# Kernel optimization log

Measured on AMD Instinct MI355X. Metric: run time of the kernel, lower is better.

## Reference

```python
import jax, jax.numpy as jnp
import numpy as np

N_STATE = 64
N_LAYERS = 4
D_MODEL = 512
D_OUT = 256
BATCH = 16
SEQLEN = 2048


def setup_inputs() -> dict:
    key = jax.random.key(0)
    ks = jax.random.split(key, 16)
    H, N, nl = D_MODEL, N_STATE, N_LAYERS
    inp = {}
    inp["x"] = jax.random.normal(ks[0], (BATCH, SEQLEN, D_MODEL), dtype=jnp.float32)
    # encoder / decoder dense
    inp["enc_w"] = jax.random.normal(ks[1], (D_MODEL, D_MODEL), jnp.float32) / np.sqrt(D_MODEL)
    inp["enc_b"] = jnp.zeros((D_MODEL,), jnp.float32)
    inp["dec_w"] = jax.random.normal(ks[2], (D_MODEL, D_OUT), jnp.float32) / np.sqrt(D_MODEL)
    inp["dec_b"] = jnp.zeros((D_OUT,), jnp.float32)
    # per-layer LayerNorm
    inp["ln_scale"] = jnp.ones((nl, D_MODEL), jnp.float32)
    inp["ln_bias"] = jnp.zeros((nl, D_MODEL), jnp.float32)
    # per-layer S4 DPLR params (stored as real/imag float pairs)
    inp["lambda_re"] = -0.5 * jnp.ones((nl, H, N), jnp.float32)
    inp["lambda_im"] = jnp.broadcast_to(np.pi * jnp.arange(N, dtype=jnp.float32), (nl, H, N))
    inp["p_re"] = jax.random.normal(ks[3], (nl, H, N), jnp.float32) * 0.5
    inp["p_im"] = jax.random.normal(ks[4], (nl, H, N), jnp.float32) * 0.5
    inp["b_re"] = jax.random.normal(ks[5], (nl, H, N), jnp.float32) * 0.5
    inp["b_im"] = jax.random.normal(ks[6], (nl, H, N), jnp.float32) * 0.5
    inp["c_re"] = jax.random.normal(ks[7], (nl, H, N), jnp.float32) * 0.5
    inp["c_im"] = jax.random.normal(ks[8], (nl, H, N), jnp.float32) * 0.5
    inp["log_step"] = jax.random.uniform(ks[9], (nl, H), jnp.float32, minval=np.log(1e-3), maxval=np.log(1e-1))
    inp["d_param"] = jnp.ones((nl, H), jnp.float32)
    # per-layer output Dense
    inp["out_w"] = jax.random.normal(ks[10], (nl, D_MODEL, D_MODEL), jnp.float32) / np.sqrt(D_MODEL)
    inp["out_b"] = jnp.zeros((nl, D_MODEL), jnp.float32)
    return inp


def _layer_norm(x, scale, bias, eps=1e-6):
    mu = jnp.mean(x, axis=-1, keepdims=True)
    var = jnp.mean(jnp.square(x - mu), axis=-1, keepdims=True)
    return (x - mu) * jax.lax.rsqrt(var + eps) * scale + bias


def _kernel_dplr(Lam, P, B, C, step, L):
    # Lam,P,B,C: [H,N] complex64; step: [H] float32 -> K: [H,L] float32
    theta = (2.0 * np.pi / L) * jnp.arange(L, dtype=jnp.float32)
    Omega = jnp.exp(-1j * theta)                        # [L] roots of unity
    g = (2.0 / step)[:, None] * ((1.0 - Omega) / (1.0 + Omega))[None, :]  # [H,L]
    c = 2.0 / (1.0 + Omega)                             # [L]
    r = 1.0 / (g[:, :, None] - Lam[:, None, :])         # [H,L,N] resolvent (Cauchy)
    Cc, Pc = jnp.conj(C), jnp.conj(P)
    k00 = jnp.einsum("hn,hln->hl", Cc * B, r)
    k01 = jnp.einsum("hn,hln->hl", Cc * P, r)
    k10 = jnp.einsum("hn,hln->hl", Pc * B, r)
    k11 = jnp.einsum("hn,hln->hl", Pc * P, r)
    at_roots = c[None, :] * (k00 - k01 * (1.0 / (1.0 + k11)) * k10)  # [H,L]
    return jnp.fft.ifft(at_roots, n=L, axis=-1).real


def _s4_apply(u, Lam, P, B, C, step, D):
    # u: [Bt,L,H]; causal FFT convolution with kernel K[h,:] per channel
    L = u.shape[1]
    K = _kernel_dplr(Lam, P, B, C, step, L)             # [H,L]
    ud = jnp.fft.rfft(u, n=2 * L, axis=1)               # [Bt,L+1,H]
    Kd = jnp.fft.rfft(K, n=2 * L, axis=-1)              # [H,L+1]
    y = jnp.fft.irfft(ud * Kd.T[None], n=2 * L, axis=1)[:, :L]
    return y + D[None, None, :] * u


def reference(x, enc_w, enc_b, ln_scale, ln_bias, lambda_re, lambda_im,
              p_re, p_im, b_re, b_im, c_re, c_im, log_step, d_param,
              out_w, out_b, dec_w, dec_b):
    h = x @ enc_w + enc_b
    n_layers = ln_scale.shape[0]
    for i in range(n_layers):
        skip = h
        z = _layer_norm(h, ln_scale[i], ln_bias[i])
        Lam = lambda_re[i] + 1j * lambda_im[i]
        P = p_re[i] + 1j * p_im[i]
        B = b_re[i] + 1j * b_im[i]
        C = c_re[i] + 1j * c_im[i]
        z = _s4_apply(z, Lam, P, B, C, jnp.exp(log_step[i]), d_param[i])
        z = jax.nn.gelu(z)
        z = z @ out_w[i] + out_b[i]
        h = skip + z  # dropout=0.0 -> identity
    logits = h @ dec_w + dec_b
    return jax.nn.log_softmax(logits, axis=-1)
```

## Files before the change

### kernel.cpp

```cpp
#include <hip/hip_runtime.h>
#include <hip/hip_bf16.h>

#define NLAY 4
#define DH   512
#define NST  64
#define NB   16
#define SL   2048
#define NDO  256
#define BL   (NB*SL)
#define KDIM 512
#define TWOPI 6.283185307179586476925287

typedef unsigned short u16;
typedef __attribute__((ext_vector_type(8))) short  short8v;
typedef __attribute__((ext_vector_type(8))) unsigned short ushort8v;
typedef __attribute__((ext_vector_type(4))) float  f32x4;

#define RCPF(x) __builtin_amdgcn_rcpf(x)

__device__ __forceinline__ float bf2f(u16 v){
  union { unsigned u; float f; } x; x.u = ((unsigned)v) << 16; return x.f;
}
__device__ __forceinline__ u16 f2bf(float f){
  union { float f; unsigned u; } x; x.f = f;
  unsigned u = x.u;
  unsigned r = u + 0x7fffu + ((u >> 16) & 1u);
  return (u16)(r >> 16);
}
__device__ __forceinline__ void cmulw(float& xr, float& xi, float wr, float wi){
  float tr = xr*wr - xi*wi;
  xi = fmaf(xr, wi, xi*wr);
  xr = tr;
}
__device__ __forceinline__ float gelu_fast(float v){
  const float c0 = 0.7978845608028654f;
  float u = c0 * fmaf(0.044715f, v*v*v, v);
  return v * RCPF(1.0f + __expf(-2.0f * u));
}

template<int SGN>
__device__ __forceinline__ void dft4w(float& r0, float& i0, float& r1, float& i1,
                                      float& r2, float& i2, float& r3, float& i3){
  const float t0r = r0 + r2, t0i = i0 + i2;
  const float t1r = r0 - r2, t1i = i0 - i2;
  const float t2r = r1 + r3, t2i = i1 + i3;
  const float t3r = r1 - r3, t3i = i1 - i3;
  r0 = t0r + t2r; i0 = t0i + t2i;
  r2 = t0r - t2r; i2 = t0i - t2i;
  if (SGN < 0){ r1 = t1r + t3i; i1 = t1i - t3r; r3 = t1r - t3i; i3 = t1i + t3r; }
  else        { r1 = t1r - t3i; i1 = t1i + t3r; r3 = t1r + t3i; i3 = t1i - t3r; }
}

template<int SGN>
__device__ __forceinline__ void dft16(float* re, float* im){
#pragma unroll
  for (int b = 0; b < 4; b++)
    dft4w<SGN>(re[b], im[b], re[4+b], im[4+b], re[8+b], im[8+b], re[12+b], im[12+b]);
  const float C1 = 0.92387953251128675613f, S1_ = 0.38268343236508977172f;
  const float C2 = 0.70710678118654752440f;
  const float sg = (SGN < 0) ? -1.f : 1.f;
  cmulw(re[5],  im[5],   C1,  sg*S1_);
  cmulw(re[9],  im[9],   C2,  sg*C2);
  cmulw(re[13], im[13],  S1_, sg*C1);
  cmulw(re[6],  im[6],   C2,  sg*C2);
  cmulw(re[10], im[10],  0.f, sg*1.f);
  cmulw(re[14], im[14], -C2,  sg*C2);
  cmulw(re[7],  im[7],   S1_, sg*C1);
  cmulw(re[11], im[11], -C2,  sg*C2);
  cmulw(re[15], im[15], -C1,  sg*(-S1_));
#pragma unroll
  for (int c = 0; c < 4; c++)
    dft4w<SGN>(re[4*c], im[4*c], re[4*c+1], im[4*c+1], re[4*c+2], im[4*c+2], re[4*c+3], im[4*c+3]);
  float tr_, ti_;
#define SWP(A,B) tr_=re[A]; re[A]=re[B]; re[B]=tr_; ti_=im[A]; im[A]=im[B]; im[B]=ti_;
  SWP(1,4) SWP(2,8) SWP(3,12) SWP(6,9) SWP(7,13) SWP(11,14)
#undef SWP
}

__device__ __forceinline__ int cxpad(int i){ return i + (i >> 4) + ((i >> 8) << 1); }
#define CXSZ 4384

__device__ __forceinline__ void fwd4096(float* re, float* im, float2* cx, int t){
  dft16<-1>(re, im);
  const float a0 = -(float)(TWOPI/4096.0) * (float)t;
#pragma unroll
  for (int k = 0; k < 16; k++){
    if (k){ float sn = __sinf(a0*(float)k), cs = __cosf(a0*(float)k); cmulw(re[k], im[k], cs, sn); }
    cx[cxpad(t + 256*k)] = make_float2(re[k], im[k]);
  }
  __syncthreads();
  const int k1 = t >> 4, m2 = t & 15;
  const int b2 = k1*256 + m2;
#pragma unroll
  for (int j = 0; j < 16; j++){ float2 v = cx[cxpad(b2 + 16*j)]; re[j] = v.x; im[j] = v.y; }
  dft16<-1>(re, im);
  const float b0 = -(float)(TWOPI/256.0) * (float)m2;
#pragma unroll
  for (int k = 0; k < 16; k++){
    if (k){ float sn = __sinf(b0*(float)k), cs = __cosf(b0*(float)k); cmulw(re[k], im[k], cs, sn); }
    cx[cxpad(b2 + 16*k)] = make_float2(re[k], im[k]);
  }
  __syncthreads();
#pragma unroll
  for (int j = 0; j < 16; j++){ float2 v = cx[cxpad(16*t + j)]; re[j] = v.x; im[j] = v.y; }
  dft16<-1>(re, im);
}

__device__ __forceinline__ void inv4096(float* re, float* im, float2* cx, int t){
  dft16<1>(re, im);
#pragma unroll
  for (int j = 0; j < 16; j++) cx[cxpad(16*t + j)] = make_float2(re[j], im[j]);
  __syncthreads();
  const int k1 = t >> 4, m2 = t & 15;
  const int b2 = k1*256 + m2;
  const float b0 = (float)(TWOPI/256.0) * (float)m2;
#pragma unroll
  for (int k = 0; k < 16; k++){
    float2 v = cx[cxpad(b2 + 16*k)];
    re[k] = v.x; im[k] = v.y;
    if (k){ float sn = __sinf(b0*(float)k), cs = __cosf(b0*(float)k); cmulw(re[k], im[k], cs, sn); }
  }
  dft16<1>(re, im);
#pragma unroll
  for (int j = 0; j < 16; j++) cx[cxpad(b2 + 16*j)] = make_float2(re[j], im[j]);
  __syncthreads();
  const float a0 = (float)(TWOPI/4096.0) * (float)t;
#pragma unroll
  for (int k = 0; k < 16; k++){
    float2 v = cx[cxpad(t + 256*k)];
    re[k] = v.x; im[k] = v.y;
    if (k){ float sn = __sinf(a0*(float)k), cs = __cosf(a0*(float)k); cmulw(re[k], im[k], cs, sn); }
  }
  dft16<1>(re, im);
}

__global__ __launch_bounds__(256) void prep_k(
  const float* __restrict__ lam_re, const float* __restrict__ lam_im,
  const float* __restrict__ p_re,  const float* __restrict__ p_im,
  const float* __restrict__ b_re,  const float* __restrict__ b_im,
  const float* __restrict__ c_re,  const float* __restrict__ c_im,
  float4* __restrict__ cwA, float4* __restrict__ cwB, float* __restrict__ cwS)
{
  const int i = blockIdx.x * 256 + threadIdx.x;
  const float lr = lam_re[i], li = lam_im[i];
  const float pr = p_re[i],  pi = p_im[i];
  const float br = b_re[i],  bi = b_im[i];
  const float cr = c_re[i],  ci = c_im[i];
  cwA[i] = make_float4(lr, li, cr*br + ci*bi, cr*bi - ci*br);
  cwB[i] = make_float4(cr*pr + ci*pi, cr*pi - ci*pr, pr*br + pi*bi, pr*bi - pi*br);
  cwS[i] = pr*pr + pi*pi;
}

__global__ __launch_bounds__(256, 2) void cauchy_k(
    const float4* __restrict__ cwA, const float4* __restrict__ cwB,
    const float* __restrict__ cwS, const float* __restrict__ lstep,
    float2* __restrict__ Kd)
{
  const int t = threadIdx.x;
  const int h = blockIdx.y, lay = blockIdx.z;
  const int lb = blockIdx.x * 256 + t;
  const int wb = (lay*DH + h) * NST;
  const float tw0 = 2.0f * expf(-lstep[lay*DH + h]);

  float T0,T1,T2,T3, g0,g1,g2,g3;
  { float sn, cs;
    sincosf((float)(TWOPI/4096.0)*(float)(lb       ), &sn, &cs); T0 = sn*RCPF(cs); g0 = tw0*T0;
    sincosf((float)(TWOPI/4096.0)*(float)(lb +  512), &sn, &cs); T1 = sn*RCPF(cs); g1 = tw0*T1;
    sincosf((float)(TWOPI/4096.0)*(float)(lb + 1024), &sn, &cs); T2 = sn*RCPF(cs); g2 = tw0*T2;
    sincosf((float)(TWOPI/4096.0)*(float)(lb + 1536), &sn, &cs); T3 = sn*RCPF(cs); g3 = tw0*T3;
  }

  float k00r0=0,k00i0=0,k01r0=0,k01i0=0,k10r0=0,k10i0=0,k11r0=0,k11i0=0;
  float k00r1=0,k00i1=0,k01r1=0,k01i1=0,k10r1=0,k10i1=0,k11r1=0,k11i1=0;
  float k00r2=0,k00i2=0,k01r2=0,k01i2=0,k10r2=0,k10i2=0,k11r2=0,k11i2=0;
  float k00r3=0,k00i3=0,k01r3=0,k01i3=0,k10r3=0,k10i3=0,k11r3=0,k11i3=0;

#pragma unroll 2
  for (int n = 0; n < NST; n++){
    const float4 A  = cwA[wb + n];
    const float4 Bv = cwB[wb + n];
    const float w11 = cwS[wb + n];
    const float nlr = -A.x;
    const float dr2 = A.x * A.x;
#define CSTEP(J) { \
    const float di = g##J - A.y; \
    const float sI = RCPF(fmaf(di, di, dr2)); \
    const float ivr = nlr * sI, ivi = -di * sI; \
    k00r##J = fmaf(A.z,  ivr, fmaf(-A.w,  ivi, k00r##J)); \
    k00i##J = fmaf(A.z,  ivi, fmaf( A.w,  ivr, k00i##J)); \
    k01r##J = fmaf(Bv.x, ivr, fmaf(-Bv.y, ivi, k01r##J)); \
    k01i##J = fmaf(Bv.x, ivi, fmaf( Bv.y, ivr, k01i##J)); \
    k10r##J = fmaf(Bv.z, ivr, fmaf(-Bv.w, ivi, k10r##J)); \
    k10i##J = fmaf(Bv.z, ivi, fmaf( Bv.w, ivr, k10i##J)); \
    k11r##J = fmaf(w11,  ivr, k11r##J); \
    k11i##J = fmaf(w11,  ivi, k11i##J); }
    CSTEP(0) CSTEP(1) CSTEP(2) CSTEP(3)
#undef CSTEP
    asm volatile("" : "+v"(k00r0), "+v"(k00r1), "+v"(k00r2), "+v"(k00r3),
                      "+v"(k11i0), "+v"(k11i1), "+v"(k11i2), "+v"(k11i3));
  }

  float2* kp = Kd + (size_t)(lay*DH + h) * 4096;
#define COUT(J, LOFF) { \
    const float d1r = 1.f + k11r##J, d1i = k11i##J; \
    const float idn = RCPF(fmaf(d1r, d1r, d1i*d1i)); \
    const float wr = k01r##J*k10r##J - k01i##J*k10i##J; \
    const float wi = k01r##J*k10i##J + k01i##J*k10r##J; \
    const float vr = fmaf(wr, d1r,  wi*d1i) * idn; \
    const float vi = fmaf(wi, d1r, -wr*d1i) * idn; \
    const float sr = k00r##J - vr, si = k00i##J - vi; \
    kp[lb + LOFF] = make_float2(fmaf(-T##J, si, sr), fmaf(T##J, sr, si)); }
  COUT(0, 0) COUT(1, 512) COUT(2, 1024) COUT(3, 1536)
#undef COUT
}

__global__ __launch_bounds__(256) void kdfft_k(float2* __restrict__ Kd){
  __shared__ float  ar[SL], ai[SL];
  __shared__ float2 cx[CXSZ];
  const int t = threadIdx.x;
  const size_t base = (size_t)blockIdx.x * 4096;
#pragma unroll
  for (int q = 0; q < 8; q++){
    const int l = t + 256*q;
    float2 v = Kd[base + l];
    const int brv = __brev((unsigned)l) >> 21;
    ar[brv] = v.x; ai[brv] = v.y;
  }
  __syncthreads();

  for (int s = 0; s < 11; s++){
    const int half = 1 << s;
    const float fac = (float)(TWOPI) / (float)(2 << s);
#pragma unroll
    for (int q = 0; q < 4; q++){
      const int v = t + 256*q;
      const int pos = v & (half - 1);
      const int i0 = ((v >> s) << (s+1)) + pos;
      const int i1 = i0 + half;
      const float ang = fac * (float)pos;
      const float wc = __cosf(ang), ws = __sinf(ang);
      const float xr = ar[i1], xi = ai[i1];
      const float tr = wc*xr - ws*xi, ti = fmaf(wc, xi, ws*xr);
      const float ur_ = ar[i0], ui_ = ai[i0];
      ar[i0] = ur_ + tr; ai[i0] = ui_ + ti;
      ar[i1] = ur_ - tr; ai[i1] = ui_ - ti;
    }
    __syncthreads();
  }

  float re[16], im[16];
#pragma unroll
  for (int j = 0; j < 16; j++){
    re[j] = (j < 8) ? ar[t + 256*j] * (1.0f/2048.f) : 0.f;
    im[j] = 0.f;
  }
  fwd4096(re, im, cx, t);
  float2* kp = Kd + base + 16*t;
#pragma unroll
  for (int k = 0; k < 16; k += 2)
    *(float4*)(kp + k) = make_float4(re[k], im[k], re[k+1], im[k+1]);
}

__global__ __launch_bounds__(256) void wconv_k(const float* __restrict__ src,
    u16* __restrict__ dst, int K, int N){
  __shared__ u16 tile[64][72];
  const size_t mb = (size_t)blockIdx.z * K * N;
  const int k0 = blockIdx.x * 64, n0 = blockIdx.y * 64;
  const int r = threadIdx.x >> 2, c4 = (threadIdx.x & 3) * 16;
  const float* s = src + mb + (size_t)(k0 + r) * N + n0 + c4;
  float4 f0 = *(const float4*)s, f1 = *(const float4*)(s+4);
  float4 f2 = *(const float4*)(s+8), f3 = *(const float4*)(s+12);
  tile[c4+0][r]=f2bf(f0.x); tile[c4+1][r]=f2bf(f0.y); tile[c4+2][r]=f2bf(f0.z); tile[c4+3][r]=f2bf(f0.w);
  tile[c4+4][r]=f2bf(f1.x); tile[c4+5][r]=f2bf(f1.y); tile[c4+6][r]=f2bf(f1.z); tile[c4+7][r]=f2bf(f1.w);
  tile[c4+8][r]=f2bf(f2.x); tile[c4+9][r]=f2bf(f2.y); tile[c4+10][r]=f2bf(f2.z); tile[c4+11][r]=f2bf(f2.w);
  tile[c4+12][r]=f2bf(f3.x); tile[c4+13][r]=f2bf(f3.y); tile[c4+14][r]=f2bf(f3.z); tile[c4+15][r]=f2bf(f3.w);
  __syncthreads();
  u16* d = dst + mb + (size_t)(n0 + r) * K + k0 + c4;
  *(ushort8v*)d       = *(const ushort8v*)&tile[r][c4];
  *(ushort8v*)(d + 8) = *(const ushort8v*)&tile[r][c4 + 8];
}

#define LTILE 32
__device__ __forceinline__ int lnswz(int h){ return ((h >> 1) + (h >> 6)) & 3; }

__global__ __launch_bounds__(256) void lnt_k(const u16* __restrict__ hsrc,
    const float* __restrict__ gam, const float* __restrict__ bet,
    u16* __restrict__ zT){
  __shared__ u16 tile[DH][LTILE];
  __shared__ float smu[LTILE], srs[LTILE];
  const int t = threadIdx.x;
  const int b = blockIdx.y, l0 = blockIdx.x * LTILE;
  const int r = t >> 3, hb = (t & 7) * 64;
  const u16* p = hsrc + ((size_t)b * SL + l0 + r) * DH + hb;
  float s = 0.f, sq = 0.f;
#pragma unroll
  for (int j8 = 0; j8 < 8; j8++){
    ushort8v w = *(const ushort8v*)(p + j8*8);
    const int h0 = hb + j8*8;
#pragma unroll
    for (int d = 0; d < 8; d++){
      const float f = bf2f((u16)w[d]);
      s += f; sq = fmaf(f, f, sq);
      tile[h0+d][r ^ (lnswz(h0+d) << 3)] = (u16)w[d];
    }
  }
  s  += __shfl_xor(s, 1);  sq += __shfl_xor(sq, 1);
  s  += __shfl_xor(s, 2);  sq += __shfl_xor(sq, 2);
  s  += __shfl_xor(s, 4);  sq += __shfl_xor(sq, 4);
  if ((t & 7) == 0){
    const float mu = s * (1.0f/DH);
    smu[r] = mu;
    srs[r] = rsqrtf(sq * (1.0f/DH) - mu*mu + 1e-6f);
  }
  __syncthreads();

#pragma unroll
  for (int hh = 0; hh < 2; hh++){
    const int h = t + hh*256;
    const float g = gam[h], be = bet[h];
    const int sw = lnswz(h);
    u16* dst = zT + ((size_t)b * DH + h) * SL + l0;
#pragma unroll
    for (int og = 0; og < 4; og++){
      const int lg = og ^ sw;
      ushort8v v = *(const ushort8v*)&tile[h][og*8];
      const float4 m0 = *(const float4*)&smu[lg*8];
      const float4 m1 = *(const float4*)&smu[lg*8 + 4];
      const float4 r0 = *(const float4*)&srs[lg*8];
      const float4 r1 = *(const float4*)&srs[lg*8 + 4];
      ushort8v o;
      o[0] = f2bf(fmaf(bf2f((u16)v[0]) - m0.x, r0.x*g, be));
      o[1] = f2bf(fmaf(bf2f((u16)v[1]) - m0.y, r0.y*g, be));
      o[2] = f2bf(fmaf(bf2f((u16)v[2]) - m0.z, r0.z*g, be));
      o[3] = f2bf(fmaf(bf2f((u16)v[3]) - m0.w, r0.w*g, be));
      o[4] = f2bf(fmaf(bf2f((u16)v[4]) - m1.x, r1.x*g, be));
      o[5] = f2bf(fmaf(bf2f((u16)v[5]) - m1.y, r1.y*g, be));
      o[6] = f2bf(fmaf(bf2f((u16)v[6]) - m1.z, r1.z*g, be));
      o[7] = f2bf(fmaf(bf2f((u16)v[7]) - m1.w, r1.w*g, be));
      *(ushort8v*)(dst + lg*8) = o;
    }
  }
}

__global__ __launch_bounds__(256) void s4conv_k(
    const u16* __restrict__ zT, const float2* __restrict__ Kd,
    const float* __restrict__ dpar, u16* __restrict__ yT)
{
  __shared__ float2 cx[CXSZ];
  const int t = threadIdx.x;
  const int wg = blockIdx.x;
  const int h = wg & 511, bp = wg >> 9;
  const u16* r1 = zT + ((size_t)(2*bp) * DH + h) * SL;
  const u16* r2 = r1 + (size_t)DH * SL;
  float ur1[8], ur2[8];
  float re[16], im[16];
#pragma unroll
  for (int j = 0; j < 8; j++){
    ur1[j] = bf2f(r1[t + 256*j]);
    ur2[j] = bf2f(r2[t + 256*j]);
    re[j] = ur1[j]; im[j] = ur2[j];
  }
#pragma unroll
  for (int j = 8; j < 16; j++){ re[j] = 0.f; im[j] = 0.f; }

  fwd4096(re, im, cx, t);

  const float2* kp = Kd + (size_t)h * 4096 + 16*t;
#pragma unroll
  for (int k = 0; k < 16; k += 2){
    float4 w2 = *(const float4*)(kp + k);
    cmulw(re[k],   im[k],   w2.x, w2.y);
    cmulw(re[k+1], im[k+1], w2.z, w2.w);
  }

  inv4096(re, im, cx, t);

  const float Dv = dpar[h];
  u16* y1 = yT + ((size_t)(2*bp) * DH + h) * SL;
  u16* y2 = y1 + (size_t)DH * SL;
#pragma unroll
  for (int j = 0; j < 8; j++){
    float v1 = fmaf(re[j], (1.0f/4096.f), Dv * ur1[j]);
    float v2 = fmaf(im[j], (1.0f/4096.f), Dv * ur2[j]);
    y1[t + 256*j] = f2bf(gelu_fast(v1));
    y2[t + 256*j] = f2bf(gelu_fast(v2));
  }
}

template<int AMODE, bool RESID, bool OUTBF>
__global__ __launch_bounds__(256) void gemm_k(
    const void* __restrict__ Aptr, const u16* __restrict__ Wt,
    const float* __restrict__ bias,
    const u16* __restrict__ resid, void* __restrict__ Coutv,
    int Mb, int N)
{
  __shared__ u16 As[128][40];
  __shared__ u16 Bs[128][40];
  const int t = threadIdx.x;
  const int n0 = blockIdx.x * 128, m0 = blockIdx.y * 128, bb = blockIdx.z;
  const int lane = t & 63, wv = t >> 6;
  const int wm = (wv >> 1) * 64, wn = (wv & 1) * 64;
  f32x4 acc[4][4];
#pragma unroll
  for (int mi = 0; mi < 4; mi++)
#pragma unroll
    for (int ni = 0; ni < 4; ni++) acc[mi][ni] = {0.f, 0.f, 0.f, 0.f};

  const u16*  Ab = (const u16*)Aptr;
  const float* Af = (const float*)Aptr;
  const size_t Abase = (AMODE == 1) ? (size_t)bb * KDIM * Mb : 0;

  for (int k0 = 0; k0 < KDIM; k0 += 32){
    __syncthreads();
    if (AMODE == 1){
      const int kk = t >> 3, ch = t & 7;
      const u16* srca = Ab + Abase + (size_t)(k0 + kk) * Mb + m0 + ch*16;
      ushort8v v0 = *(const ushort8v*)srca;
      ushort8v v1 = *(const ushort8v*)(srca + 8);
      const int col = (kk & 7) | (((kk >> 3) ^ (ch & 3)) << 3);
#pragma unroll
      for (int i = 0; i < 8; i++){
        As[ch*16 + i][col]     = (u16)v0[i];
        As[ch*16 + 8 + i][col] = (u16)v1[i];
      }
    } else if (AMODE == 0){
      const int r = t >> 1, kh = (t & 1) << 4;
      const u16* srca = Ab + (size_t)(m0 + r) * KDIM + k0 + kh;
      ushort8v v0 = *(const ushort8v*)srca;
      ushort8v v1 = *(const ushort8v*)(srca + 8);
      const int s3 = (r >> 4) & 3;
      const int c0 = (((kh >> 3) ^ s3) << 3);
      const int c1 = ((((kh >> 3) + 1) ^ s3) << 3);
      *(ushort8v*)&As[r][c0] = v0;
      *(ushort8v*)&As[r][c1] = v1;
    } else {
      const int r = t >> 1, kh = (t & 1) << 4;
      const float* sf = Af + (size_t)(m0 + r) * KDIM + k0 + kh;
      float4 f0 = *(const float4*)sf,     f1 = *(const float4*)(sf + 4);
      float4 f2 = *(const float4*)(sf+8), f3 = *(const float4*)(sf + 12);
      ushort8v v0, v1;
      v0[0]=f2bf(f0.x); v0[1]=f2bf(f0.y); v0[2]=f2bf(f0.z); v0[3]=f2bf(f0.w);
      v0[4]=f2bf(f1.x); v0[5]=f2bf(f1.y); v0[6]=f2bf(f1.z); v0[7]=f2bf(f1.w);
      v1[0]=f2bf(f2.x); v1[1]=f2bf(f2.y); v1[2]=f2bf(f2.z); v1[3]=f2bf(f2.w);
      v1[4]=f2bf(f3.x); v1[5]=f2bf(f3.y); v1[6]=f2bf(f3.z); v1[7]=f2bf(f3.w);
      const int s3 = (r >> 4) & 3;
      const int c0 = (((kh >> 3) ^ s3) << 3);
      const int c1 = ((((kh >> 3) + 1) ^ s3) << 3);
      *(ushort8v*)&As[r][c0] = v0;
      *(ushort8v*)&As[r][c1] = v1;
    }
    {
      const int r = t >> 1, kh = (t & 1) << 4;
      const u16* srcb = Wt + (size_t)(n0 + r) * KDIM + k0 + kh;
      ushort8v v0 = *(const ushort8v*)srcb;
      ushort8v v1 = *(const ushort8v*)(srcb + 8);
      const int s3 = (r >> 4) & 3;
      const int c0 = (((kh >> 3) ^ s3) << 3);
      const int c1 = ((((kh >> 3) + 1) ^ s3) << 3);
      *(ushort8v*)&Bs[r][c0] = v0;
      *(ushort8v*)&Bs[r][c1] = v1;
    }
    __syncthreads();

    const int ko = (lane >> 4) * 8;
    const int fr = lane & 15;
    short8v af[4], bf[4];
#pragma unroll
    for (int mi = 0; mi < 4; mi++){
      const int col = (((ko >> 3) ^ (((wm >> 4) + mi) & 3)) << 3);
      af[mi] = *(const short8v*)&As[wm + mi*16 + fr][col];
    }
#pragma unroll
    for (int ni = 0; ni < 4; ni++){
      const int col = (((ko >> 3) ^ (((wn >> 4) + ni) & 3)) << 3);
      bf[ni] = *(const short8v*)&Bs[wn + ni*16 + fr][col];
    }
#pragma unroll
    for (int mi = 0; mi < 4; mi++)
#pragma unroll
      for (int ni = 0; ni < 4; ni++)
        acc[mi][ni] = __builtin_amdgcn_mfma_f32_16x16x32_bf16(af[mi], bf[ni], acc[mi][ni], 0, 0, 0);
  }

  const int fr = lane & 15;
  const int rq = (lane >> 4) * 4;
#pragma unroll
  for (int mi = 0; mi < 4; mi++){
#pragma unroll
    for (int ni = 0; ni < 4; ni++){
      const int gn = n0 + wn + ni*16 + fr;
      const float bs = bias[gn];
#pragma unroll
      for (int q = 0; q < 4; q++){
        const int gm = m0 + wm + mi*16 + rq + q;
        const size_t idx = ((size_t)bb * Mb + gm) * N + gn;
        float v = acc[mi][ni][q] + bs;
        if (RESID) v += bf2f(resid[idx]);
        if (OUTBF) ((u16*)Coutv)[idx] = f2bf(v);
        else       ((float*)Coutv)[idx] = v;
      }
    }
  }
}

__global__ __launch_bounds__(256) void lsm_k(float* __restrict__ o){
  const int row = blockIdx.x * 4 + (threadIdx.x >> 6);
  const int lane = threadIdx.x & 63;
  float* p = o + (size_t)row * NDO + lane * 4;
  float4 v = *(const float4*)p;
  float mx = fmaxf(fmaxf(v.x, v.y), fmaxf(v.z, v.w));
#pragma unroll
  for (int q = 32; q; q >>= 1) mx = fmaxf(mx, __shfl_xor(mx, q));
  float e = __expf(v.x - mx) + __expf(v.y - mx) + __expf(v.z - mx) + __expf(v.w - mx);
#pragma unroll
  for (int q = 32; q; q >>= 1) e += __shfl_xor(e, q);
  const float lse = mx + __logf(e);
  v.x -= lse; v.y -= lse; v.z -= lse; v.w -= lse;
  *(float4*)p = v;
}

extern "C" void kernel_launch(void* const* d_in, const int* in_sizes, int n_in,
                              void* d_out, int out_size, void* d_ws, size_t ws_size,
                              hipStream_t stream)
{
  (void)in_sizes; (void)n_in; (void)out_size; (void)ws_size;
  const float* x      = (const float*)d_in[0];
  const float* enc_w  = (const float*)d_in[1];
  const float* enc_b  = (const float*)d_in[2];
  const float* dec_w  = (const float*)d_in[3];
  const float* dec_b  = (const float*)d_in[4];
  const float* ln_s   = (const float*)d_in[5];
  const float* ln_b   = (const float*)d_in[6];
  const float* lam_re = (const float*)d_in[7];
  const float* lam_im = (const float*)d_in[8];
  const float* p_re   = (const float*)d_in[9];
  const float* p_im   = (const float*)d_in[10];
  const float* b_re   = (const float*)d_in[11];
  const float* b_im   = (const float*)d_in[12];
  const float* c_re   = (const float*)d_in[13];
  const float* c_im   = (const float*)d_in[14];
  const float* lstep  = (const float*)d_in[15];
  const float* d_par  = (const float*)d_in[16];
  const float* out_w  = (const float*)d_in[17];
  const float* out_b  = (const float*)d_in[18];

  char* ws = (char*)d_ws;
  u16*    hbuf = (u16*)(ws);
  u16*    zT   = (u16*)  (ws + (size_t)67108864 + 33554432);
  u16*    yT   = (u16*)  (ws + (size_t)67108864 + 2*33554432);
  float2* Kd   = (float2*)(ws + (size_t)67108864 + 3*33554432);
  u16*    Wt   = (u16*)  (ws + (size_t)67108864 + 3*33554432 + 67108864);
  u16*    WtEnc = Wt;
  u16*    WtOut = Wt + 262144;
  u16*    WtDec = Wt + 262144*5;
  float*  outp = (float*)d_out;

  float4* cwA = (float4*)d_out;
  float4* cwB = cwA + 131072;
  float*  cwS = (float*)(cwB + 131072);

  prep_k<<<dim3(NLAY*DH*NST/256), 256, 0, stream>>>(lam_re, lam_im, p_re, p_im,
                                                    b_re, b_im, c_re, c_im, cwA, cwB, cwS);
  wconv_k<<<dim3(8, 8, 1), 256, 0, stream>>>(enc_w, WtEnc, KDIM, DH);
  wconv_k<<<dim3(8, 8, NLAY), 256, 0, stream>>>(out_w, WtOut, KDIM, DH);
  wconv_k<<<dim3(8, 4, 1), 256, 0, stream>>>(dec_w, WtDec, KDIM, NDO);
  cauchy_k<<<dim3(2, DH, NLAY), 256, 0, stream>>>(cwA, cwB, cwS, lstep, Kd);
  kdfft_k<<<dim3(NLAY*DH), 256, 0, stream>>>(Kd);
  gemm_k<2,false,true><<<dim3(DH/128, BL/128, 1), 256, 0, stream>>>(
      x, WtEnc, enc_b, nullptr, hbuf, BL, DH);
  for (int i = 0; i < NLAY; i++){
    lnt_k<<<dim3(SL/LTILE, NB), 256, 0, stream>>>(hbuf, ln_s + i*DH, ln_b + i*DH, zT);
    s4conv_k<<<dim3((NB/2)*DH), 256, 0, stream>>>(
        zT, Kd + (size_t)i*DH*4096, d_par + i*DH, yT);
    gemm_k<1,true,true><<<dim3(DH/128, SL/128, NB), 256, 0, stream>>>(
        yT, WtOut + (size_t)i*262144, out_b + i*DH, hbuf, hbuf, SL, DH);
  }
  gemm_k<0,false,false><<<dim3(NDO/128, BL/128, 1), 256, 0, stream>>>(
      hbuf, WtDec, dec_b, nullptr, outp, BL, NDO);
  lsm_k<<<dim3(BL/4), 256, 0, stream>>>(outp);
}
```

Before: 780.1 us.

## Load GEMM tiles with direct global-to-LDS loads and a new swizzled layout

The GEMM now stages the weight tile, and the A tile in bf16 row-major mode, with global_load_lds 16-byte transfers that write straight into shared memory instead of going through registers. Shared tiles become flat unpadded 4096-element arrays using a row-XOR swizzle, and every load and fragment read is rewritten to that layout. The FFT helpers get extra barriers that fix read-after-write hazards on reused shared buffers, and an asm register-pinning hint in the kernel-generation loop is removed. The aim is less VGPR traffic and fewer instructions per tile load, at the cost of a few added syncs in the FFTs.

Result: slower. 831.6 us (+6.6%).

```diff
diff --git a/kernel.cpp b/kernel.cpp
--- a/kernel.cpp
+++ b/kernel.cpp
@@ -36,6 +36,11 @@
   const float c0 = 0.7978845608028654f;
   float u = c0 * fmaf(0.044715f, v*v*v, v);
   return v * RCPF(1.0f + __expf(-2.0f * u));
+}
+__device__ __forceinline__ void gload16(const void* g, void* l){
+  __builtin_amdgcn_global_load_lds(
+      (__attribute__((address_space(1))) void*)(g),
+      (__attribute__((address_space(3))) void*)(l), 16, 0, 0);
 }
 
 template<int SGN>
@@ -95,6 +100,7 @@
   for (int j = 0; j < 16; j++){ float2 v = cx[cxpad(b2 + 16*j)]; re[j] = v.x; im[j] = v.y; }
   dft16<-1>(re, im);
   const float b0 = -(float)(TWOPI/256.0) * (float)m2;
+  __syncthreads();
 #pragma unroll
   for (int k = 0; k < 16; k++){
     if (k){ float sn = __sinf(b0*(float)k), cs = __cosf(b0*(float)k); cmulw(re[k], im[k], cs, sn); }
@@ -121,6 +127,7 @@
     if (k){ float sn = __sinf(b0*(float)k), cs = __cosf(b0*(float)k); cmulw(re[k], im[k], cs, sn); }
   }
   dft16<1>(re, im);
+  __syncthreads();
 #pragma unroll
   for (int j = 0; j < 16; j++) cx[cxpad(b2 + 16*j)] = make_float2(re[j], im[j]);
   __syncthreads();
@@ -196,8 +203,6 @@
     k11i##J = fmaf(w11,  ivi, k11i##J); }
     CSTEP(0) CSTEP(1) CSTEP(2) CSTEP(3)
 #undef CSTEP
-    asm volatile("" : "+v"(k00r0), "+v"(k00r1), "+v"(k00r2), "+v"(k00r3),
-                      "+v"(k11i0), "+v"(k11i1), "+v"(k11i2), "+v"(k11i3));
   }
 
   float2* kp = Kd + (size_t)(lay*DH + h) * 4096;
@@ -394,12 +399,13 @@
     const u16* __restrict__ resid, void* __restrict__ Coutv,
     int Mb, int N)
 {
-  __shared__ u16 As[128][40];
-  __shared__ u16 Bs[128][40];
+  __shared__ u16 As[4096];
+  __shared__ u16 Bs[4096];
   const int t = threadIdx.x;
   const int n0 = blockIdx.x * 128, m0 = blockIdx.y * 128, bb = blockIdx.z;
   const int lane = t & 63, wv = t >> 6;
   const int wm = (wv >> 1) * 64, wn = (wv & 1) * 64;
+  const int wbase = t & 192;
   f32x4 acc[4][4];
 #pragma unroll
   for (int mi = 0; mi < 4; mi++)
@@ -412,27 +418,28 @@
 
   for (int k0 = 0; k0 < KDIM; k0 += 32){
     __syncthreads();
-    if (AMODE == 1){
+    if (AMODE == 0){
+#pragma unroll
+      for (int i = 0; i < 2; i++){
+        const int G = i*256 + t;
+        const int r = G >> 2;
+        const int g = ((G & 3) ^ r ^ (r >> 2)) & 3;
+        gload16(Ab + (size_t)(m0 + r) * KDIM + k0 + g*8,
+                As + (size_t)(i*256 + wbase) * 8);
+      }
+    } else if (AMODE == 1){
       const int kk = t >> 3, ch = t & 7;
       const u16* srca = Ab + Abase + (size_t)(k0 + kk) * Mb + m0 + ch*16;
       ushort8v v0 = *(const ushort8v*)srca;
       ushort8v v1 = *(const ushort8v*)(srca + 8);
-      const int col = (kk & 7) | (((kk >> 3) ^ (ch & 3)) << 3);
+      const int gsl = kk >> 3, ko7 = kk & 7;
 #pragma unroll
       for (int i = 0; i < 8; i++){
-        As[ch*16 + i][col]     = (u16)v0[i];
-        As[ch*16 + 8 + i][col] = (u16)v1[i];
+        int m = ch*16 + i;
+        As[(size_t)((m<<2) | ((gsl ^ m ^ (m>>2)) & 3))*8 + ko7] = (u16)v0[i];
+        m += 8;
+        As[(size_t)((m<<2) | ((gsl ^ m ^ (m>>2)) & 3))*8 + ko7] = (u16)v1[i];
       }
-    } else if (AMODE == 0){
-      const int r = t >> 1, kh = (t & 1) << 4;
-      const u16* srca = Ab + (size_t)(m0 + r) * KDIM + k0 + kh;
-      ushort8v v0 = *(const ushort8v*)srca;
-      ushort8v v1 = *(const ushort8v*)(srca + 8);
-      const int s3 = (r >> 4) & 3;
-      const int c0 = (((kh >> 3) ^ s3) << 3);
-      const int c1 = ((((kh >> 3) + 1) ^ s3) << 3);
-      *(ushort8v*)&As[r][c0] = v0;
-      *(ushort8v*)&As[r][c1] = v1;
     } else {
       const int r = t >> 1, kh = (t & 1) << 4;
       const float* sf = Af + (size_t)(m0 + r) * KDIM + k0 + kh;
@@ -443,37 +450,31 @@
       v0[4]=f2bf(f1.x); v0[5]=f2bf(f1.y); v0[6]=f2bf(f1.z); v0[7]=f2bf(f1.w);
       v1[0]=f2bf(f2.x); v1[1]=f2bf(f2.y); v1[2]=f2bf(f2.z); v1[3]=f2bf(f2.w);
       v1[4]=f2bf(f3.x); v1[5]=f2bf(f3.y); v1[6]=f2bf(f3.z); v1[7]=f2bf(f3.w);
-      const int s3 = (r >> 4) & 3;
-      const int c0 = (((kh >> 3) ^ s3) << 3);
-      const int c1 = ((((kh >> 3) + 1) ^ s3) << 3);
-      *(ushort8v*)&As[r][c0] = v0;
-      *(ushort8v*)&As[r][c1] = v1;
-    }
-    {
-      const int r = t >> 1, kh = (t & 1) << 4;
-      const u16* srcb = Wt + (size_t)(n0 + r) * KDIM + k0 + kh;
-      ushort8v v0 = *(const ushort8v*)srcb;
-      ushort8v v1 = *(const ushort8v*)(srcb + 8);
-      const int s3 = (r >> 4) & 3;
-      const int c0 = (((kh >> 3) ^ s3) << 3);
-      const int c1 = ((((kh >> 3) + 1) ^ s3) << 3);
-      *(ushort8v*)&Bs[r][c0] = v0;
-      *(ushort8v*)&Bs[r][c1] = v1;
+      const int key = (r ^ (r >> 2)) & 3;
+      *(ushort8v*)&As[(size_t)((r<<2) | ((kh>>3) ^ key))*8]       = v0;
+      *(ushort8v*)&As[(size_t)((r<<2) | (((kh>>3)+1) ^ key))*8]   = v1;
+    }
+#pragma unroll
+    for (int i = 0; i < 2; i++){
+      const int G = i*256 + t;
+      const int r = G >> 2;
+      const int g = ((G & 3) ^ r ^ (r >> 2)) & 3;
+      gload16(Wt + (size_t)(n0 + r) * KDIM + k0 + g*8,
+              Bs + (size_t)(i*256 + wbase) * 8);
     }
     __syncthreads();
 
-    const int ko = (lane >> 4) * 8;
-    const int fr = lane & 15;
+    const int fr = lane & 15, g4 = lane >> 4;
     short8v af[4], bf[4];
 #pragma unroll
     for (int mi = 0; mi < 4; mi++){
-      const int col = (((ko >> 3) ^ (((wm >> 4) + mi) & 3)) << 3);
-      af[mi] = *(const short8v*)&As[wm + mi*16 + fr][col];
+      const int r = wm + mi*16 + fr;
+      af[mi] = *(const short8v*)&As[(size_t)((r<<2) | ((g4 ^ r ^ (r>>2)) & 3)) * 8];
     }
 #pragma unroll
     for (int ni = 0; ni < 4; ni++){
-      const int col = (((ko >> 3) ^ (((wn >> 4) + ni) & 3)) << 3);
-      bf[ni] = *(const short8v*)&Bs[wn + ni*16 + fr][col];
+      const int r = wn + ni*16 + fr;
+      bf[ni] = *(const short8v*)&Bs[(size_t)((r<<2) | ((g4 ^ r ^ (r>>2)) & 3)) * 8];
     }
 #pragma unroll
     for (int mi = 0; mi < 4; mi++)
```
